# Performance work log

Hardware: AMD Instinct MI355X
Metric: run time of the kernel (lower is better)

Reference implementation:

```python
import jax, jax.numpy as jnp
import numpy as np

N_HEADS = 8
HEAD_DIM = 48  # d_model 384 / 8 heads
D_MODEL = 384


def setup_inputs() -> dict:
    key = jax.random.key(0)
    k1, k2, k3, k4, k5 = jax.random.split(key, 5)
    B, S = 8, 2048
    return {
        "x": jax.random.normal(k1, (B, S, D_MODEL), dtype=jnp.float32),
        "W_qkv": jax.random.normal(k2, (3 * D_MODEL, D_MODEL), dtype=jnp.float32) * 0.02,
        "b_qkv": jax.random.normal(k3, (3 * D_MODEL,), dtype=jnp.float32) * 0.02,
        "W_o": jax.random.normal(k4, (D_MODEL, D_MODEL), dtype=jnp.float32) * 0.02,
        "b_o": jax.random.normal(k5, (D_MODEL,), dtype=jnp.float32) * 0.02,
    }


def reference(x, W_qkv, b_qkv, W_o, b_o):
    B, S, D = x.shape
    H, hd = N_HEADS, HEAD_DIM
    # fused QKV projection: [B,S,3D]
    qkv = jnp.einsum("bsd,ed->bse", x, W_qkv) + b_qkv
    # [B,S,H,3*hd] -> [B,H,S,3*hd]
    qkv = qkv.reshape(B, S, H, 3 * hd).transpose(0, 2, 1, 3)
    Q, K, V = jnp.split(qkv, 3, axis=-1)  # each [B,H,S,hd]
    scale = 1.0 / np.sqrt(hd).astype(np.float32)
    scores = jnp.einsum("bhqd,bhkd->bhqk", Q, K) * scale  # [B,H,S,S]
    # NOTE: original softmaxes over dim=1 (heads), not the key dim
    attn = jax.nn.softmax(scores, axis=1)
    values = jnp.einsum("bhqk,bhkd->bhqd", attn, V)  # [B,H,S,hd]
    # NOTE: original reshapes [B,H,S,hd] directly to [B,S,H*hd] (no permute back)
    values = values.reshape(B, S, H * hd)
    out = jnp.einsum("bsd,ed->bse", values, W_o) + b_o
    return out
```

## Files before the change

kernel.cpp:

```cpp
#include <hip/hip_runtime.h>
#include <hip/hip_bf16.h>

#define BB 8
#define SS 2048
#define DD 384
#define HH 8
#define HD 48
#define QT 32
#define KT 32

typedef unsigned short u16;
typedef unsigned int u32;
typedef unsigned short u16x4 __attribute__((ext_vector_type(4)));
typedef unsigned short u16x8 __attribute__((ext_vector_type(8)));
typedef short s16x8 __attribute__((ext_vector_type(8)));
typedef float f32x4 __attribute__((ext_vector_type(4)));

__device__ __forceinline__ float bf2f(u16 v){
  union { u32 u; float f; } x; x.u = ((u32)v) << 16; return x.f;
}
__device__ __forceinline__ u16 f2bf(float f){
  union { float f; u32 u; } x; x.f = f;
  u32 r = x.u + 0x7fffu + ((x.u >> 16) & 1u);
  return (u16)(r >> 16);
}
__device__ __forceinline__ void split2(float f, u16& h, u16& l){
  union { float f; u32 u; } x; x.f = f;
  h = (u16)(x.u >> 16);
  l = f2bf(f - bf2f(h));
}
__device__ __forceinline__ u32 pack_trunc2(float a, float b){
  union { float f; u32 u; } xa, xb; xa.f = a; xb.f = b;
  return (xa.u >> 16) | (xb.u & 0xffff0000u);
}

#define LBAR() do { \
  asm volatile("s_waitcnt lgkmcnt(0)" ::: "memory"); \
  __builtin_amdgcn_s_barrier(); \
  asm volatile("" ::: "memory"); \
} while (0)

__global__ __launch_bounds__(512, 4) void qkv_gemm(
    const float* __restrict__ x, const float* __restrict__ W,
    const float* __restrict__ bias,
    u16* __restrict__ Q, u16* __restrict__ Kd, u16* __restrict__ Vt)
{
  __shared__ u16 Ah[128][40], Al[128][40], Bh[128][40], Bl[128][40];
  const int tid  = threadIdx.x;
  const int w    = tid >> 6, lane = tid & 63;
  const int lg   = lane >> 4, ln = lane & 15;
  const int wm   = w >> 1, wn = w & 1;
  const int mb   = blockIdx.x / 9, nb = blockIdx.x % 9;
  const int m0   = mb * 128, n0 = nb * 128;
  const int srow = tid >> 3, sk4 = (tid & 7) << 2;
  const float qscale = 0.2082350972f;

  f32x4 acc[8];
  #pragma unroll
  for (int i = 0; i < 8; i++) acc[i] = (f32x4){0.f,0.f,0.f,0.f};

  for (int ks = 0; ks < 12; ks++){
    const int k0 = ks * 32;
    __syncthreads();
    #pragma unroll
    for (int p = 0; p < 2; p++){
      const int row = srow + p*64;
      float4 av = *(const float4*)(x + (long)(m0+row)*DD + k0 + sk4);
      float4 bv = *(const float4*)(W + (long)(n0+row)*DD + k0 + sk4);
      u16 h0,l0,h1,l1,h2,l2,h3,l3;
      split2(av.x,h0,l0); split2(av.y,h1,l1); split2(av.z,h2,l2); split2(av.w,h3,l3);
      *(u16x4*)&Ah[row][sk4] = (u16x4){h0,h1,h2,h3};
      *(u16x4*)&Al[row][sk4] = (u16x4){l0,l1,l2,l3};
      split2(bv.x,h0,l0); split2(bv.y,h1,l1); split2(bv.z,h2,l2); split2(bv.w,h3,l3);
      *(u16x4*)&Bh[row][sk4] = (u16x4){h0,h1,h2,h3};
      *(u16x4*)&Bl[row][sk4] = (u16x4){l0,l1,l2,l3};
    }
    __syncthreads();
    s16x8 bh[4], bl[4];
    #pragma unroll
    for (int fn = 0; fn < 4; fn++){
      const int br = wn*64 + fn*16 + ln;
      bh[fn] = *(const s16x8*)&Bh[br][lg*8];
      bl[fn] = *(const s16x8*)&Bl[br][lg*8];
    }
    #pragma unroll
    for (int fm = 0; fm < 2; fm++){
      const int ar = wm*32 + fm*16 + ln;
      s16x8 ah = *(const s16x8*)&Ah[ar][lg*8];
      s16x8 al = *(const s16x8*)&Al[ar][lg*8];
      #pragma unroll
      for (int fn = 0; fn < 4; fn++){
        f32x4 c = acc[fm*4+fn];
        c = __builtin_amdgcn_mfma_f32_16x16x32_bf16(ah, bh[fn], c, 0, 0, 0);
        c = __builtin_amdgcn_mfma_f32_16x16x32_bf16(ah, bl[fn], c, 0, 0, 0);
        c = __builtin_amdgcn_mfma_f32_16x16x32_bf16(al, bh[fn], c, 0, 0, 0);
        acc[fm*4+fn] = c;
      }
    }
  }
  #pragma unroll
  for (int fm = 0; fm < 2; fm++){
    #pragma unroll
    for (int fn = 0; fn < 4; fn++){
      const int e = n0 + wn*64 + fn*16 + ln;
      const float bi = bias[e];
      const int h = e / 144, c = e % 144;
      #pragma unroll
      for (int r = 0; r < 4; r++){
        const int mm = m0 + wm*32 + fm*16 + lg*4 + r;
        const int bb = mm >> 11, s = mm & 2047;
        const float v = acc[fm*4+fn][r] + bi;
        if (c < 48){
          Q[(((long)(bb*HH + h))*SS + s)*HD + c] = f2bf(v * qscale);
        } else if (c < 96){
          Kd[(((long)(bb*HH + h))*SS + s)*HD + (c-48)] = f2bf(v);
        } else {
          Vt[(((long)(bb*HH + h))*HD + (c-96))*SS + s] = f2bf(v);
        }
      }
    }
  }
}

__global__ __launch_bounds__(512, 4) void attn_kernel(
    const u16* __restrict__ Q, const u16* __restrict__ K,
    const u16* __restrict__ Vg, float* __restrict__ vals)
{
  __shared__ u16 Ss[2][HH][QT][36];
  __shared__ u16 Pb[2][HH][QT][40];

  const int tid  = threadIdx.x;
  const int h    = tid >> 6;
  const int lane = tid & 63;
  const int wg   = ((int)blockIdx.x % 8) * 64 + (int)blockIdx.x / 8;
  const int b    = wg >> 6;
  const int qt   = wg & 63;
  const int q0   = qt * QT;
  const int lg   = lane >> 4;
  const int ln   = lane & 15;

  const long hbase = ((long)(b*HH + h)) * SS;
  const u16* vbase = Vg + ((long)(b*HH + h)) * HD * SS;
  const s16x8 z8 = (s16x8){0,0,0,0,0,0,0,0};

  s16x8 qf0[2], qf1[2];
  #pragma unroll
  for (int qs = 0; qs < 2; qs++){
    const u16* qp = Q + (hbase + q0 + qs*16 + ln)*HD;
    qf0[qs] = *(const s16x8*)(qp + lg*8);
    if (lane < 32) qf1[qs] = *(const s16x8*)(qp + 32 + lg*8);
    else           qf1[qs] = z8;
  }

  f32x4 oacc[2][3];
  #pragma unroll
  for (int qs = 0; qs < 2; qs++)
    #pragma unroll
    for (int c = 0; c < 3; c++) oacc[qs][c] = (f32x4){0.f,0.f,0.f,0.f};

  const int smq = tid >> 4, smk = (tid & 15) << 1;

#define QKT(cbx, k0x) { \
    __builtin_amdgcn_s_setprio(1); \
    _Pragma("unroll") \
    for (int nt = 0; nt < 2; nt++){ \
      const u16* kp = K + (hbase + (k0x) + nt*16 + ln)*HD; \
      s16x8 kf0 = *(const s16x8*)(kp + lg*8); \
      s16x8 kf1; \
      if (lane < 32) kf1 = *(const s16x8*)(kp + 32 + lg*8); \
      else           kf1 = z8; \
      _Pragma("unroll") \
      for (int qs = 0; qs < 2; qs++){ \
        f32x4 a = (f32x4){0.f,0.f,0.f,0.f}; \
        a = __builtin_amdgcn_mfma_f32_16x16x32_bf16(kf0, qf0[qs], a, 0, 0, 0); \
        a = __builtin_amdgcn_mfma_f32_16x16x32_bf16(kf1, qf1[qs], a, 0, 0, 0); \
        u32 w0 = pack_trunc2(a[0], a[1]); \
        u32 w1 = pack_trunc2(a[2], a[3]); \
        u32* dst = (u32*)&Ss[cbx][h][qs*16 + ln][nt*16 + lg*4]; \
        dst[0] = w0; dst[1] = w1; \
      } \
    } \
    __builtin_amdgcn_s_setprio(0); \
  }

  QKT(0, 0)
  LBAR();

  int cb = 0, k0 = 0;
  for (int t = 0; t < SS/KT; t++){
    s16x8 vf0 = *(const s16x8*)(vbase + (long)(     ln)*SS + k0 + lg*8);
    s16x8 vf1 = *(const s16x8*)(vbase + (long)(16 + ln)*SS + k0 + lg*8);
    s16x8 vf2 = *(const s16x8*)(vbase + (long)(32 + ln)*SS + k0 + lg*8);

    if (t < SS/KT - 1) QKT(cb^1, k0 + KT)

    {
      float e0[8], e1[8];
      float sum0 = 0.f, sum1 = 0.f;
      #pragma unroll
      for (int hh = 0; hh < 8; hh++){
        u32 wv = *(const u32*)&Ss[cb][hh][smq][smk];
        union { u32 u; float f; } a0, a1;
        a0.u = wv << 16; a1.u = wv & 0xffff0000u;
        e0[hh] = __builtin_amdgcn_exp2f(a0.f);
        e1[hh] = __builtin_amdgcn_exp2f(a1.f);
        sum0 += e0[hh]; sum1 += e1[hh];
      }
      float r0 = __builtin_amdgcn_rcpf(sum0);
      float r1 = __builtin_amdgcn_rcpf(sum1);
      #pragma unroll
      for (int hh = 0; hh < 8; hh++)
        *(u32*)&Pb[cb][hh][smq][smk] = pack_trunc2(e0[hh]*r0, e1[hh]*r1);
    }

    LBAR();

    __builtin_amdgcn_s_setprio(1);
    #pragma unroll
    for (int qs = 0; qs < 2; qs++){
      s16x8 pf = *(const s16x8*)&Pb[cb][h][qs*16 + ln][lg*8];
      oacc[qs][0] = __builtin_amdgcn_mfma_f32_16x16x32_bf16(pf, vf0, oacc[qs][0], 0, 0, 0);
      oacc[qs][1] = __builtin_amdgcn_mfma_f32_16x16x32_bf16(pf, vf1, oacc[qs][1], 0, 0, 0);
      oacc[qs][2] = __builtin_amdgcn_mfma_f32_16x16x32_bf16(pf, vf2, oacc[qs][2], 0, 0, 0);
    }
    __builtin_amdgcn_s_setprio(0);

    cb ^= 1; k0 += KT;
  }
#undef QKT

  float* op = vals + (hbase + q0)*HD;
  #pragma unroll
  for (int qs = 0; qs < 2; qs++)
    #pragma unroll
    for (int c = 0; c < 3; c++)
      #pragma unroll
      for (int r = 0; r < 4; r++)
        op[(long)(qs*16 + lg*4 + r)*HD + c*16 + ln] = oacc[qs][c][r];
}

__global__ __launch_bounds__(512, 4) void out_gemm(
    const float* __restrict__ A, const float* __restrict__ W,
    const float* __restrict__ bias, float* __restrict__ out)
{
  __shared__ u16 Ah[128][40], Al[128][40], Bh[128][40], Bl[128][40];
  const int tid  = threadIdx.x;
  const int w    = tid >> 6, lane = tid & 63;
  const int lg   = lane >> 4, ln = lane & 15;
  const int wm   = w >> 1, wn = w & 1;
  const int mb   = blockIdx.x / 3, nb = blockIdx.x % 3;
  const int m0   = mb * 128, n0 = nb * 128;
  const int srow = tid >> 3, sk4 = (tid & 7) << 2;

  f32x4 acc[8];
  #pragma unroll
  for (int i = 0; i < 8; i++) acc[i] = (f32x4){0.f,0.f,0.f,0.f};

  for (int ks = 0; ks < 12; ks++){
    const int k0 = ks * 32;
    __syncthreads();
    #pragma unroll
    for (int p = 0; p < 2; p++){
      const int row = srow + p*64;
      float4 av = *(const float4*)(A + (long)(m0+row)*DD + k0 + sk4);
      float4 bv = *(const float4*)(W + (long)(n0+row)*DD + k0 + sk4);
      u16 h0,l0,h1,l1,h2,l2,h3,l3;
      split2(av.x,h0,l0); split2(av.y,h1,l1); split2(av.z,h2,l2); split2(av.w,h3,l3);
      *(u16x4*)&Ah[row][sk4] = (u16x4){h0,h1,h2,h3};
      *(u16x4*)&Al[row][sk4] = (u16x4){l0,l1,l2,l3};
      split2(bv.x,h0,l0); split2(bv.y,h1,l1); split2(bv.z,h2,l2); split2(bv.w,h3,l3);
      *(u16x4*)&Bh[row][sk4] = (u16x4){h0,h1,h2,h3};
      *(u16x4*)&Bl[row][sk4] = (u16x4){l0,l1,l2,l3};
    }
    __syncthreads();
    s16x8 bh[4], bl[4];
    #pragma unroll
    for (int fn = 0; fn < 4; fn++){
      const int br = wn*64 + fn*16 + ln;
      bh[fn] = *(const s16x8*)&Bh[br][lg*8];
      bl[fn] = *(const s16x8*)&Bl[br][lg*8];
    }
    #pragma unroll
    for (int fm = 0; fm < 2; fm++){
      const int ar = wm*32 + fm*16 + ln;
      s16x8 ah = *(const s16x8*)&Ah[ar][lg*8];
      s16x8 al = *(const s16x8*)&Al[ar][lg*8];
      #pragma unroll
      for (int fn = 0; fn < 4; fn++){
        f32x4 c = acc[fm*4+fn];
        c = __builtin_amdgcn_mfma_f32_16x16x32_bf16(ah, bh[fn], c, 0, 0, 0);
        c = __builtin_amdgcn_mfma_f32_16x16x32_bf16(ah, bl[fn], c, 0, 0, 0);
        c = __builtin_amdgcn_mfma_f32_16x16x32_bf16(al, bh[fn], c, 0, 0, 0);
        acc[fm*4+fn] = c;
      }
    }
  }
  #pragma unroll
  for (int fm = 0; fm < 2; fm++){
    #pragma unroll
    for (int fn = 0; fn < 4; fn++){
      const int e = n0 + wn*64 + fn*16 + ln;
      const float bi = bias[e];
      #pragma unroll
      for (int r = 0; r < 4; r++){
        const int mm = m0 + wm*32 + fm*16 + lg*4 + r;
        out[(long)mm*DD + e] = acc[fm*4+fn][r] + bi;
      }
    }
  }
}

extern "C" void kernel_launch(void* const* d_in, const int* in_sizes, int n_in,
                              void* d_out, int out_size, void* d_ws, size_t ws_size,
                              hipStream_t stream)
{
  const float* x    = (const float*)d_in[0];
  const float* Wqkv = (const float*)d_in[1];
  const float* bqkv = (const float*)d_in[2];
  const float* Wo   = (const float*)d_in[3];
  const float* bo   = (const float*)d_in[4];
  float* out = (float*)d_out;

  const size_t QSZ = (size_t)BB*HH*SS*HD;
  u16* Q  = (u16*)d_ws;
  u16* K  = Q + QSZ;
  u16* Vt = K + QSZ;
  float* vals = (float*)(Vt + QSZ);

  qkv_gemm<<<1152, 512, 0, stream>>>(x, Wqkv, bqkv, Q, K, Vt);
  attn_kernel<<<512, 512, 0, stream>>>(Q, K, Vt, vals);
  out_gemm<<<384, 512, 0, stream>>>(vals, Wo, bo, out);
}
```

Baseline: 249.9 us.

## Pre-split inputs to bf16 hi/lo, widen attention key tile, drop double buffering

A new prep kernel splits x, W_qkv and W_o into bf16 high/low halves once. The QKV GEMM then loads pre-split bf16 data with a register prefetch of the next k-slice, and the output GEMM loads pre-split weights directly. The attention kernel moves from a 32-key to a 64-key tile with a single shared buffer and no longer overlaps the next tile's QK^T with the current softmax. The extra prep pass adds roughly 2x the x traffic in writes plus reads, and removing the double buffer may expose latency.

Result: faster. 236.3 us (-5.4%).

```diff
diff --git a/kernel.cpp b/kernel.cpp
--- a/kernel.cpp
+++ b/kernel.cpp
@@ -7,12 +7,13 @@
 #define HH 8
 #define HD 48
 #define QT 32
-#define KT 32
+#define KT 64
 
 typedef unsigned short u16;
 typedef unsigned int u32;
 typedef unsigned short u16x4 __attribute__((ext_vector_type(4)));
 typedef unsigned short u16x8 __attribute__((ext_vector_type(8)));
+typedef unsigned int u32x2 __attribute__((ext_vector_type(2)));
 typedef short s16x8 __attribute__((ext_vector_type(8)));
 typedef float f32x4 __attribute__((ext_vector_type(4)));
 
@@ -40,8 +41,31 @@
   asm volatile("" ::: "memory"); \
 } while (0)
 
-__global__ __launch_bounds__(512, 4) void qkv_gemm(
-    const float* __restrict__ x, const float* __restrict__ W,
+__global__ __launch_bounds__(256) void split_prep(
+    const float* __restrict__ x, const float* __restrict__ Wq,
+    const float* __restrict__ Wo,
+    u16* __restrict__ xh, u16* __restrict__ xl,
+    u16* __restrict__ wqh, u16* __restrict__ wql,
+    u16* __restrict__ woh, u16* __restrict__ wol)
+{
+  const int N1 = (BB*SS*DD)/4, N2 = (3*DD*DD)/4, N3 = (DD*DD)/4;
+  for (int i = blockIdx.x*blockDim.x + threadIdx.x; i < N1+N2+N3;
+       i += gridDim.x*blockDim.x){
+    const float4* src; u16 *dh, *dl; int off;
+    if (i < N1){ src = (const float4*)x; dh = xh; dl = xl; off = i; }
+    else if (i < N1+N2){ src = (const float4*)Wq; dh = wqh; dl = wql; off = i-N1; }
+    else { src = (const float4*)Wo; dh = woh; dl = wol; off = i-N1-N2; }
+    float4 v = src[off];
+    u16 h0,l0,h1,l1,h2,l2,h3,l3;
+    split2(v.x,h0,l0); split2(v.y,h1,l1); split2(v.z,h2,l2); split2(v.w,h3,l3);
+    *(u16x4*)(dh + (long)off*4) = (u16x4){h0,h1,h2,h3};
+    *(u16x4*)(dl + (long)off*4) = (u16x4){l0,l1,l2,l3};
+  }
+}
+
+__global__ __launch_bounds__(512, 4) void qkv_gemm2(
+    const u16* __restrict__ xh, const u16* __restrict__ xl,
+    const u16* __restrict__ Wh, const u16* __restrict__ Wl,
     const float* __restrict__ bias,
     u16* __restrict__ Q, u16* __restrict__ Kd, u16* __restrict__ Vt)
 {
@@ -52,30 +76,37 @@
   const int wm   = w >> 1, wn = w & 1;
   const int mb   = blockIdx.x / 9, nb = blockIdx.x % 9;
   const int m0   = mb * 128, n0 = nb * 128;
-  const int srow = tid >> 3, sk4 = (tid & 7) << 2;
+  const int sr   = tid >> 2, so = (tid & 3) << 3;
   const float qscale = 0.2082350972f;
 
+  const u16* pah = xh + (long)(m0+sr)*DD + so;
+  const u16* pal = xl + (long)(m0+sr)*DD + so;
+  const u16* pbh = Wh + (long)(n0+sr)*DD + so;
+  const u16* pbl = Wl + (long)(n0+sr)*DD + so;
+
+  u16x8 ra = *(const u16x8*)(pah);
+  u16x8 rl = *(const u16x8*)(pal);
+  u16x8 rb = *(const u16x8*)(pbh);
+  u16x8 rc = *(const u16x8*)(pbl);
+
   f32x4 acc[8];
   #pragma unroll
   for (int i = 0; i < 8; i++) acc[i] = (f32x4){0.f,0.f,0.f,0.f};
 
   for (int ks = 0; ks < 12; ks++){
-    const int k0 = ks * 32;
-    __syncthreads();
-    #pragma unroll
-    for (int p = 0; p < 2; p++){
-      const int row = srow + p*64;
-      float4 av = *(const float4*)(x + (long)(m0+row)*DD + k0 + sk4);
-      float4 bv = *(const float4*)(W + (long)(n0+row)*DD + k0 + sk4);
-      u16 h0,l0,h1,l1,h2,l2,h3,l3;
-      split2(av.x,h0,l0); split2(av.y,h1,l1); split2(av.z,h2,l2); split2(av.w,h3,l3);
-      *(u16x4*)&Ah[row][sk4] = (u16x4){h0,h1,h2,h3};
-      *(u16x4*)&Al[row][sk4] = (u16x4){l0,l1,l2,l3};
-      split2(bv.x,h0,l0); split2(bv.y,h1,l1); split2(bv.z,h2,l2); split2(bv.w,h3,l3);
-      *(u16x4*)&Bh[row][sk4] = (u16x4){h0,h1,h2,h3};
-      *(u16x4*)&Bl[row][sk4] = (u16x4){l0,l1,l2,l3};
-    }
-    __syncthreads();
+    LBAR();
+    *(u16x8*)&Ah[sr][so] = ra;
+    *(u16x8*)&Al[sr][so] = rl;
+    *(u16x8*)&Bh[sr][so] = rb;
+    *(u16x8*)&Bl[sr][so] = rc;
+    LBAR();
+    if (ks < 11){
+      const int k1 = (ks+1) * 32;
+      ra = *(const u16x8*)(pah + k1);
+      rl = *(const u16x8*)(pal + k1);
+      rb = *(const u16x8*)(pbh + k1);
+      rc = *(const u16x8*)(pbl + k1);
+    }
     s16x8 bh[4], bl[4];
     #pragma unroll
     for (int fn = 0; fn < 4; fn++){
@@ -110,13 +141,9 @@
         const int mm = m0 + wm*32 + fm*16 + lg*4 + r;
         const int bb = mm >> 11, s = mm & 2047;
         const float v = acc[fm*4+fn][r] + bi;
-        if (c < 48){
-          Q[(((long)(bb*HH + h))*SS + s)*HD + c] = f2bf(v * qscale);
-        } else if (c < 96){
-          Kd[(((long)(bb*HH + h))*SS + s)*HD + (c-48)] = f2bf(v);
-        } else {
-          Vt[(((long)(bb*HH + h))*HD + (c-96))*SS + s] = f2bf(v);
-        }
+        if (c < 48)       Q[(((long)(bb*HH + h))*SS + s)*HD + c] = f2bf(v * qscale);
+        else if (c < 96)  Kd[(((long)(bb*HH + h))*SS + s)*HD + (c-48)] = f2bf(v);
+        else              Vt[(((long)(bb*HH + h))*HD + (c-96))*SS + s] = f2bf(v);
       }
     }
   }
@@ -126,8 +153,8 @@
     const u16* __restrict__ Q, const u16* __restrict__ K,
     const u16* __restrict__ Vg, float* __restrict__ vals)
 {
-  __shared__ u16 Ss[2][HH][QT][36];
-  __shared__ u16 Pb[2][HH][QT][40];
+  __shared__ u16 Ss[HH][QT][72];
+  __shared__ u16 Pb[HH][QT][72];
 
   const int tid  = threadIdx.x;
   const int h    = tid >> 6;
@@ -158,76 +185,84 @@
     #pragma unroll
     for (int c = 0; c < 3; c++) oacc[qs][c] = (f32x4){0.f,0.f,0.f,0.f};
 
-  const int smq = tid >> 4, smk = (tid & 15) << 1;
-
-#define QKT(cbx, k0x) { \
-    __builtin_amdgcn_s_setprio(1); \
-    _Pragma("unroll") \
-    for (int nt = 0; nt < 2; nt++){ \
-      const u16* kp = K + (hbase + (k0x) + nt*16 + ln)*HD; \
-      s16x8 kf0 = *(const s16x8*)(kp + lg*8); \
-      s16x8 kf1; \
-      if (lane < 32) kf1 = *(const s16x8*)(kp + 32 + lg*8); \
-      else           kf1 = z8; \
-      _Pragma("unroll") \
-      for (int qs = 0; qs < 2; qs++){ \
-        f32x4 a = (f32x4){0.f,0.f,0.f,0.f}; \
-        a = __builtin_amdgcn_mfma_f32_16x16x32_bf16(kf0, qf0[qs], a, 0, 0, 0); \
-        a = __builtin_amdgcn_mfma_f32_16x16x32_bf16(kf1, qf1[qs], a, 0, 0, 0); \
-        u32 w0 = pack_trunc2(a[0], a[1]); \
-        u32 w1 = pack_trunc2(a[2], a[3]); \
-        u32* dst = (u32*)&Ss[cbx][h][qs*16 + ln][nt*16 + lg*4]; \
-        dst[0] = w0; dst[1] = w1; \
-      } \
-    } \
-    __builtin_amdgcn_s_setprio(0); \
-  }
-
-  QKT(0, 0)
-  LBAR();
-
-  int cb = 0, k0 = 0;
+  const int smq = tid >> 4, smk4 = (tid & 15) << 2;
+
   for (int t = 0; t < SS/KT; t++){
-    s16x8 vf0 = *(const s16x8*)(vbase + (long)(     ln)*SS + k0 + lg*8);
-    s16x8 vf1 = *(const s16x8*)(vbase + (long)(16 + ln)*SS + k0 + lg*8);
-    s16x8 vf2 = *(const s16x8*)(vbase + (long)(32 + ln)*SS + k0 + lg*8);
-
-    if (t < SS/KT - 1) QKT(cb^1, k0 + KT)
+    const int k0 = t * KT;
+
+    s16x8 vf[3][2];
+    #pragma unroll
+    for (int c = 0; c < 3; c++)
+      #pragma unroll
+      for (int ksub = 0; ksub < 2; ksub++)
+        vf[c][ksub] = *(const s16x8*)(vbase + (long)(c*16 + ln)*SS + k0 + ksub*32 + lg*8);
+
+    s16x8 kfA[4], kfB[4];
+    #pragma unroll
+    for (int nt = 0; nt < 4; nt++){
+      const u16* kp = K + (hbase + k0 + nt*16 + ln)*HD;
+      kfA[nt] = *(const s16x8*)(kp + lg*8);
+      if (lane < 32) kfB[nt] = *(const s16x8*)(kp + 32 + lg*8);
+      else           kfB[nt] = z8;
+    }
+
+    __builtin_amdgcn_s_setprio(1);
+    #pragma unroll
+    for (int nt = 0; nt < 4; nt++){
+      #pragma unroll
+      for (int qs = 0; qs < 2; qs++){
+        f32x4 a = (f32x4){0.f,0.f,0.f,0.f};
+        a = __builtin_amdgcn_mfma_f32_16x16x32_bf16(kfA[nt], qf0[qs], a, 0, 0, 0);
+        a = __builtin_amdgcn_mfma_f32_16x16x32_bf16(kfB[nt], qf1[qs], a, 0, 0, 0);
+        u32x2 pw; pw[0] = pack_trunc2(a[0], a[1]); pw[1] = pack_trunc2(a[2], a[3]);
+        *(u32x2*)&Ss[h][qs*16 + ln][nt*16 + lg*4] = pw;
+      }
+    }
+    __builtin_amdgcn_s_setprio(0);
+    LBAR();
 
     {
-      float e0[8], e1[8];
-      float sum0 = 0.f, sum1 = 0.f;
+      float e0[8], e1[8], e2[8], e3[8];
+      float s0 = 0.f, s1 = 0.f, s2 = 0.f, s3 = 0.f;
       #pragma unroll
       for (int hh = 0; hh < 8; hh++){
-        u32 wv = *(const u32*)&Ss[cb][hh][smq][smk];
-        union { u32 u; float f; } a0, a1;
-        a0.u = wv << 16; a1.u = wv & 0xffff0000u;
+        u32x2 wv = *(const u32x2*)&Ss[hh][smq][smk4];
+        union { u32 u; float f; } a0, a1, a2, a3;
+        a0.u = wv[0] << 16; a1.u = wv[0] & 0xffff0000u;
+        a2.u = wv[1] << 16; a3.u = wv[1] & 0xffff0000u;
         e0[hh] = __builtin_amdgcn_exp2f(a0.f);
         e1[hh] = __builtin_amdgcn_exp2f(a1.f);
-        sum0 += e0[hh]; sum1 += e1[hh];
-      }
-      float r0 = __builtin_amdgcn_rcpf(sum0);
-      float r1 = __builtin_amdgcn_rcpf(sum1);
-      #pragma unroll
-      for (int hh = 0; hh < 8; hh++)
-        *(u32*)&Pb[cb][hh][smq][smk] = pack_trunc2(e0[hh]*r0, e1[hh]*r1);
-    }
-
+        e2[hh] = __builtin_amdgcn_exp2f(a2.f);
+        e3[hh] = __builtin_amdgcn_exp2f(a3.f);
+        s0 += e0[hh]; s1 += e1[hh]; s2 += e2[hh]; s3 += e3[hh];
+      }
+      float r0 = __builtin_amdgcn_rcpf(s0);
+      float r1 = __builtin_amdgcn_rcpf(s1);
+      float r2 = __builtin_amdgcn_rcpf(s2);
+      float r3 = __builtin_amdgcn_rcpf(s3);
+      #pragma unroll
+      for (int hh = 0; hh < 8; hh++){
+        u32x2 pw;
+        pw[0] = pack_trunc2(e0[hh]*r0, e1[hh]*r1);
+        pw[1] = pack_trunc2(e2[hh]*r2, e3[hh]*r3);
+        *(u32x2*)&Pb[hh][smq][smk4] = pw;
+      }
+    }
     LBAR();
 
     __builtin_amdgcn_s_setprio(1);
     #pragma unroll
     for (int qs = 0; qs < 2; qs++){
-      s16x8 pf = *(const s16x8*)&Pb[cb][h][qs*16 + ln][lg*8];
-      oacc[qs][0] = __builtin_amdgcn_mfma_f32_16x16x32_bf16(pf, vf0, oacc[qs][0], 0, 0, 0);
-      oacc[qs][1] = __builtin_amdgcn_mfma_f32_16x16x32_bf16(pf, vf1, oacc[qs][1], 0, 0, 0);
-      oacc[qs][2] = __builtin_amdgcn_mfma_f32_16x16x32_bf16(pf, vf2, oacc[qs][2], 0, 0, 0);
+      #pragma unroll
+      for (int ksub = 0; ksub < 2; ksub++){
+        s16x8 pf = *(const s16x8*)&Pb[h][qs*16 + ln][ksub*32 + lg*8];
+        oacc[qs][0] = __builtin_amdgcn_mfma_f32_16x16x32_bf16(pf, vf[0][ksub], oacc[qs][0], 0, 0, 0);
+        oacc[qs][1] = __builtin_amdgcn_mfma_f32_16x16x32_bf16(pf, vf[1][ksub], oacc[qs][1], 0, 0, 0);
+        oacc[qs][2] = __builtin_amdgcn_mfma_f32_16x16x32_bf16(pf, vf[2][ksub], oacc[qs][2], 0, 0, 0);
+      }
     }
     __builtin_amdgcn_s_setprio(0);
-
-    cb ^= 1; k0 += KT;
-  }
-#undef QKT
+  }
 
   float* op = vals + (hbase + q0)*HD;
   #pragma unroll
@@ -239,8 +274,9 @@
         op[(long)(qs*16 + lg*4 + r)*HD + c*16 + ln] = oacc[qs][c][r];
 }
 
-__global__ __launch_bounds__(512, 4) void out_gemm(
-    const float* __restrict__ A, const float* __restrict__ W,
+__global__ __launch_bounds__(512, 4) void out_gemm2(
+    const float* __restrict__ A,
+    const u16* __restrict__ Wh, const u16* __restrict__ Wl,
     const float* __restrict__ bias, float* __restrict__ out)
 {
   __shared__ u16 Ah[128][40], Al[128][40], Bh[128][40], Bl[128][40];
@@ -251,6 +287,7 @@
   const int mb   = blockIdx.x / 3, nb = blockIdx.x % 3;
   const int m0   = mb * 128, n0 = nb * 128;
   const int srow = tid >> 3, sk4 = (tid & 7) << 2;
+  const int sr2  = tid >> 2, so2 = (tid & 3) << 3;
 
   f32x4 acc[8];
   #pragma unroll
@@ -263,15 +300,13 @@
     for (int p = 0; p < 2; p++){
       const int row = srow + p*64;
       float4 av = *(const float4*)(A + (long)(m0+row)*DD + k0 + sk4);
-      float4 bv = *(const float4*)(W + (long)(n0+row)*DD + k0 + sk4);
       u16 h0,l0,h1,l1,h2,l2,h3,l3;
       split2(av.x,h0,l0); split2(av.y,h1,l1); split2(av.z,h2,l2); split2(av.w,h3,l3);
       *(u16x4*)&Ah[row][sk4] = (u16x4){h0,h1,h2,h3};
       *(u16x4*)&Al[row][sk4] = (u16x4){l0,l1,l2,l3};
-      split2(bv.x,h0,l0); split2(bv.y,h1,l1); split2(bv.z,h2,l2); split2(bv.w,h3,l3);
-      *(u16x4*)&Bh[row][sk4] = (u16x4){h0,h1,h2,h3};
-      *(u16x4*)&Bl[row][sk4] = (u16x4){l0,l1,l2,l3};
-    }
+    }
+    *(u16x8*)&Bh[sr2][so2] = *(const u16x8*)(Wh + (long)(n0+sr2)*DD + k0 + so2);
+    *(u16x8*)&Bl[sr2][so2] = *(const u16x8*)(Wl + (long)(n0+sr2)*DD + k0 + so2);
     __syncthreads();
     s16x8 bh[4], bl[4];
     #pragma unroll
@@ -321,13 +356,22 @@
   const float* bo   = (const float*)d_in[4];
   float* out = (float*)d_out;
 
-  const size_t QSZ = (size_t)BB*HH*SS*HD;
-  u16* Q  = (u16*)d_ws;
-  u16* K  = Q + QSZ;
-  u16* Vt = K + QSZ;
-  float* vals = (float*)(Vt + QSZ);
-
-  qkv_gemm<<<1152, 512, 0, stream>>>(x, Wqkv, bqkv, Q, K, Vt);
+  const size_t QSZ  = (size_t)BB*HH*SS*HD;
+  const size_t WQSZ = (size_t)3*DD*DD;
+  const size_t WOSZ = (size_t)DD*DD;
+  u16* Q   = (u16*)d_ws;
+  u16* K   = Q + QSZ;
+  u16* Vt  = K + QSZ;
+  u16* xh  = Vt + QSZ;
+  u16* xl  = xh + QSZ;
+  float* vals = (float*)xh;
+  u16* wqh = xl + QSZ;
+  u16* wql = wqh + WQSZ;
+  u16* woh = wql + WQSZ;
+  u16* wol = woh + WOSZ;
+
+  split_prep<<<2048, 256, 0, stream>>>(x, Wqkv, Wo, xh, xl, wqh, wql, woh, wol);
+  qkv_gemm2<<<1152, 512, 0, stream>>>(xh, xl, wqh, wql, bqkv, Q, K, Vt);
   attn_kernel<<<512, 512, 0, stream>>>(Q, K, Vt, vals);
-  out_gemm<<<384, 512, 0, stream>>>(vals, Wo, bo, out);
-}
+  out_gemm2<<<384, 512, 0, stream>>>(vals, woh, wol, bo, out);
+}
```
